# Optimization experiments

Hardware: AMD Instinct MI355X
Metric: run time of the kernel (lower is better)

Reference implementation:

```python
import jax, jax.numpy as jnp
import numpy as np


def setup_inputs() -> dict:
    key = jax.random.key(0)
    kx, ka, kb, kc, kw, ke = jax.random.split(key, 6)
    B, T = 4096, 8192
    x = jax.random.normal(kx, (B, T), dtype=jnp.float32)
    a = jax.random.uniform(ka, (1,), jnp.float32, 0.95, 0.999)
    b = jax.random.uniform(kb, (1,), jnp.float32, -0.5, 0.5)
    c = jax.random.uniform(kc, (1,), jnp.float32, -0.1, 0.1)
    w = jax.random.uniform(kw, (1,), jnp.float32, -0.5, 0.5)
    e = jax.random.uniform(ke, (1,), jnp.float32, -0.1, 0.1)
    return {"x": x, "a": a, "b": b, "c": c, "w": w, "e": e}


def reference(x, a, b, c, w, e):
    # x: [B, T]; a,b,c,w,e: [1] scalar params.
    # Linear recurrence h_t = a*h_{t-1} + b*x_t + c, h_{-1}=0; output z = w*h_T + e.
    h0 = jnp.zeros((x.shape[0],), dtype=x.dtype)  # [B]

    def step(h, xt):
        return a * h + b * xt + c, None

    hT, _ = jax.lax.scan(step, h0, x.T)  # scan over T, carry [B]
    return w * hT + e  # [B]
```

## Files before the change

### kernel.cpp

```cpp
#include <hip/hip_runtime.h>


constexpr int T_LEN = 8192;
constexpr int BLOCK = 256;
constexpr int ROWS_PER_BLOCK = BLOCK / 64;
constexpr int CHUNKS = T_LEN / (64 * 4);

typedef float vfloat4 __attribute__((ext_vector_type(4)));

__global__ __launch_bounds__(BLOCK) void recur_row_kernel(
    const float* __restrict__ x,
    const float* __restrict__ pa, const float* __restrict__ pb,
    const float* __restrict__ pc, const float* __restrict__ pw,
    const float* __restrict__ pe, float* __restrict__ out)
{
    const int wid  = threadIdx.x >> 6;
    const int lane = threadIdx.x & 63;
    const int row  = blockIdx.x * ROWS_PER_BLOCK + wid;

    const float a = pa[0];
    const float b = pb[0];
    const float c = pc[0];
    const float w = pw[0];
    const float e = pe[0];

    const double ad = (double)a;
    double a256d = ad;
    #pragma unroll
    for (int i = 0; i < 8; ++i) a256d *= a256d;
    const float A256 = (float)a256d;

    int expn = 4 * (63 - lane);
    double wgt_d = 1.0, base = ad;
    while (expn) { if (expn & 1) wgt_d *= base; base *= base; expn >>= 1; }
    const float wgt = (float)wgt_d;

    const vfloat4* xr = reinterpret_cast<const vfloat4*>(x + (size_t)row * T_LEN);
    float p = 0.0f;
    #pragma unroll
    for (int u = 0; u < CHUNKS; ++u) {
        vfloat4 v = __builtin_nontemporal_load(&xr[u * 64 + lane]);
        float q = ((v.x * a + v.y) * a + v.z) * a + v.w;
        p = A256 * p + q;
    }
    float part = wgt * p;

    #pragma unroll
    for (int off = 32; off > 0; off >>= 1)
        part += __shfl_down(part, off, 64);

    if (lane == 0) {
        double a8192 = a256d * a256d;
        a8192 *= a8192;
        a8192 *= a8192;
        a8192 *= a8192;
        a8192 *= a8192;
        double S = (1.0 - a8192) / (1.0 - ad);
        out[row] = w * (b * part + c * (float)S) + e;
    }
}

extern "C" void kernel_launch(void* const* d_in, const int* in_sizes, int n_in,
                              void* d_out, int out_size, void* d_ws, size_t ws_size,
                              hipStream_t stream) {
    const float* x  = (const float*)d_in[0];
    const float* pa = (const float*)d_in[1];
    const float* pb = (const float*)d_in[2];
    const float* pc = (const float*)d_in[3];
    const float* pw = (const float*)d_in[4];
    const float* pe = (const float*)d_in[5];
    float* out = (float*)d_out;

    const int B = out_size;
    recur_row_kernel<<<dim3(B / ROWS_PER_BLOCK), dim3(BLOCK), 0, stream>>>(
        x, pa, pb, pc, pw, pe, out);
}
```

Before: 24.49 us.

## Split each row across two wavefronts and combine halves via shared memory

Each row's time axis is now split into two halves, each processed by its own wavefront, so there are twice as many waves in flight and each wave's serial chain is half as long. The two partial sums are combined through shared memory using a^4096 scaling. Nontemporal loads are also replaced with plain loads. The cost is a block-wide barrier and a shared-memory step, and the kernel stays memory-bound at 128 MB of input.

```diff
diff --git a/kernel.cpp b/kernel.cpp
--- a/kernel.cpp
+++ b/kernel.cpp
@@ -2,9 +2,10 @@
 
 
 constexpr int T_LEN = 8192;
-constexpr int BLOCK = 256;
-constexpr int ROWS_PER_BLOCK = BLOCK / 64;
-constexpr int CHUNKS = T_LEN / (64 * 4);
+constexpr int BLOCK = 512;
+constexpr int ROWS_PER_BLOCK = 4;
+constexpr int HALF = T_LEN / 2;
+constexpr int CHUNKS = HALF / (64 * 4);
 
 typedef float vfloat4 __attribute__((ext_vector_type(4)));
 
@@ -14,9 +15,11 @@
     const float* __restrict__ pc, const float* __restrict__ pw,
     const float* __restrict__ pe, float* __restrict__ out)
 {
-    const int wid  = threadIdx.x >> 6;
-    const int lane = threadIdx.x & 63;
-    const int row  = blockIdx.x * ROWS_PER_BLOCK + wid;
+    const int wid   = threadIdx.x >> 6;
+    const int lane  = threadIdx.x & 63;
+    const int rloc  = wid >> 1;
+    const int half  = wid & 1;
+    const int row   = blockIdx.x * ROWS_PER_BLOCK + rloc;
 
     const float a = pa[0];
     const float b = pb[0];
@@ -35,11 +38,12 @@
     while (expn) { if (expn & 1) wgt_d *= base; base *= base; expn >>= 1; }
     const float wgt = (float)wgt_d;
 
-    const vfloat4* xr = reinterpret_cast<const vfloat4*>(x + (size_t)row * T_LEN);
+    const vfloat4* xr = reinterpret_cast<const vfloat4*>(
+        x + (size_t)row * T_LEN + (size_t)half * HALF);
     float p = 0.0f;
     #pragma unroll
     for (int u = 0; u < CHUNKS; ++u) {
-        vfloat4 v = __builtin_nontemporal_load(&xr[u * 64 + lane]);
+        vfloat4 v = xr[u * 64 + lane];
         float q = ((v.x * a + v.y) * a + v.z) * a + v.w;
         p = A256 * p + q;
     }
@@ -49,14 +53,20 @@
     for (int off = 32; off > 0; off >>= 1)
         part += __shfl_down(part, off, 64);
 
-    if (lane == 0) {
-        double a8192 = a256d * a256d;
-        a8192 *= a8192;
-        a8192 *= a8192;
-        a8192 *= a8192;
-        a8192 *= a8192;
+    __shared__ float sred[8];
+    if (lane == 0) sred[wid] = part;
+    __syncthreads();
+
+    if (threadIdx.x < ROWS_PER_BLOCK) {
+        const int r = threadIdx.x;
+        double a4096 = a256d * a256d;
+        a4096 *= a4096;
+        a4096 *= a4096;
+        a4096 *= a4096;
+        double a8192 = a4096 * a4096;
         double S = (1.0 - a8192) / (1.0 - ad);
-        out[row] = w * (b * part + c * (float)S) + e;
+        float D = (float)a4096 * sred[2 * r] + sred[2 * r + 1];
+        out[blockIdx.x * ROWS_PER_BLOCK + r] = w * (b * D + c * (float)S) + e;
     }
 }
 
```

Result: slower. 26.15 us (+6.8%).
